# Optimization experiments

Hardware: AMD Instinct MI355X
Metric: run time of the kernel (lower is better)

Reference implementation:

```python
import jax, jax.numpy as jnp
import numpy as np

N_NODES = 100000
N_EDGES = 1600000
D_IN = 128
H1 = 128           # hidden_channels
H2 = int(H1 * 0.6) # 76, per int(hidden_channels * 0.6)
D_OUT = 64


def setup_inputs() -> dict:
    key = jax.random.key(0)
    ks = jax.random.split(key, 12)
    def lin(k, fan_in, fan_out):
        # torch Linear default init: U(-1/sqrt(fan_in), 1/sqrt(fan_in)); stored as [in, out]
        bound = 1.0 / np.sqrt(fan_in)
        return jax.random.uniform(k, (fan_in, fan_out), jnp.float32, -bound, bound)
    x = jax.random.normal(ks[0], (N_NODES, D_IN), jnp.float32)
    edge_index = jax.random.randint(ks[1], (2, N_EDGES), 0, N_NODES, dtype=jnp.int64)
    return {
        "x": x,
        "edge_index": edge_index,
        "Wl1": lin(ks[2], D_IN, H1),  "Wr1": lin(ks[3], D_IN, H1),
        "b1": jnp.zeros((H1,), jnp.float32),
        "Wl2": lin(ks[4], H1, H2),    "Wr2": lin(ks[5], H1, H2),
        "b2": jnp.zeros((H2,), jnp.float32),
        "Wl3": lin(ks[6], H2, D_OUT), "Wr3": lin(ks[7], H2, D_OUT),
        "b3": jnp.zeros((D_OUT,), jnp.float32),
    }


def reference(x, edge_index, Wl1, Wr1, b1, Wl2, Wr2, b2, Wl3, Wr3, b3):
    src, dst = edge_index[0], edge_index[1]
    n = x.shape[0]
    # in-degree of each target node (mean aggregation denominator), clamped to 1
    deg = jax.ops.segment_sum(jnp.ones_like(src, dtype=x.dtype), dst, num_segments=n)
    inv_deg = (1.0 / jnp.maximum(deg, 1.0))[:, None]

    def sage(h, Wl, Wr, b):
        # gather source features, scatter-add to targets, mean, then dual linear
        agg = jax.ops.segment_sum(h[src], dst, num_segments=n) * inv_deg
        return agg @ Wl + h @ Wr + b  # lin_l(mean_j x_j) + lin_r(x_i) + bias

    h = jax.nn.relu(sage(x, Wl1, Wr1, b1))
    h = jax.nn.relu(sage(h, Wl2, Wr2, b2))
    return sage(h, Wl3, Wr3, b3)
```

## Files before the change

kernel.cpp:

```cpp
#include <hip/hip_runtime.h>
#include <hip/hip_bf16.h>
#include <cstdint>
#include <cstddef>


typedef __attribute__((ext_vector_type(8))) short bf16x8;
typedef __attribute__((ext_vector_type(4))) float f32x4;

__device__ __forceinline__ short f2bf(float f) {
  uint32_t u = __builtin_bit_cast(uint32_t, f);
  u += 0x7fffu + ((u >> 16) & 1u);
  return (short)(u >> 16);
}
__device__ __forceinline__ float bflo(uint32_t u) {
  union { uint32_t i; float f; } v; v.i = u << 16; return v.f;
}
__device__ __forceinline__ float bfhi(uint32_t u) {
  union { uint32_t i; float f; } v; v.i = u & 0xffff0000u; return v.f;
}

__global__ void k_detect(const int* __restrict__ ei, int* __restrict__ flag, int E) {
  int t = threadIdx.x;
  int stride = E / 4096; if (stride < 1) stride = 1;
  int found = 0;
  for (int i = t; i < 4096; i += 256) {
    long long e = (long long)i * stride;
    if (e < E && ei[2 * e + 1] != 0) found = 1;
  }
  if (found) atomicOr(flag, 1);
}

__device__ __forceinline__ int edge_val(const int* ei, int is64, size_t pos) {
  return is64 ? ei[2 * pos] : ei[pos];
}

#define GPART 256

__global__ __launch_bounds__(256)
void k_bhist(const int* __restrict__ ei, const int* __restrict__ flag,
             int* __restrict__ hist, int E, int NB, int CPB) {
  __shared__ int lh[1024];
  int g = blockIdx.x, t = threadIdx.x;
  for (int b = t; b < NB; b += 256) lh[b] = 0;
  __syncthreads();
  int is64 = (*flag == 0);
  int e0 = g * CPB, e1 = min(e0 + CPB, E);
  for (int e = e0 + t; e < e1; e += 256) {
    int d = edge_val(ei, is64, (size_t)E + e);
    atomicAdd(&lh[d >> 7], 1);
  }
  __syncthreads();
  for (int b = t; b < NB; b += 256) hist[(size_t)g * NB + b] = lh[b];
}

__global__ void k_csum(const int* __restrict__ hist, int* __restrict__ total,
                       int NB, int G) {
  int b = blockIdx.x, t = threadIdx.x;
  int s = 0;
  for (int g = t; g < G; g += 64) s += hist[(size_t)g * NB + b];
  for (int off = 32; off; off >>= 1) s += __shfl_down(s, off);
  if (t == 0) total[b] = s;
}

__global__ void k_bscan(const int* __restrict__ total, int* __restrict__ bbase,
                        int NB) {
  __shared__ int sh[1024];
  int t = threadIdx.x;
  int v = (t < NB) ? total[t] : 0;
  sh[t] = v; __syncthreads();
  for (int off = 1; off < 1024; off <<= 1) {
    int x = (t >= off) ? sh[t - off] : 0;
    __syncthreads();
    sh[t] += x;
    __syncthreads();
  }
  if (t < NB) bbase[t] = sh[t] - v;
  if (t == NB - 1) bbase[NB] = sh[t];
}

__global__ void k_coff(int* __restrict__ hist, const int* __restrict__ bbase,
                       int NB, int G) {
  int b = blockIdx.x, t = threadIdx.x;
  int carry = bbase[b];
  for (int g0 = 0; g0 < G; g0 += 64) {
    int v = hist[(size_t)(g0 + t) * NB + b];
    int incl = v;
    #pragma unroll
    for (int off = 1; off < 64; off <<= 1) {
      int x = __shfl_up(incl, off);
      if (t >= off) incl += x;
    }
    hist[(size_t)(g0 + t) * NB + b] = carry + incl - v;
    carry += __shfl(incl, 63);
  }
}

__global__ __launch_bounds__(256)
void k_bscatter(const int* __restrict__ ei, const int* __restrict__ flag,
                const int* __restrict__ off, uint32_t* __restrict__ staging,
                int E, int NB, int CPB) {
  __shared__ int lcur[1024];
  int g = blockIdx.x, t = threadIdx.x;
  for (int b = t; b < NB; b += 256) lcur[b] = off[(size_t)g * NB + b];
  __syncthreads();
  int is64 = (*flag == 0);
  int e0 = g * CPB, e1 = min(e0 + CPB, E);
  for (int e = e0 + t; e < e1; e += 256) {
    int s = edge_val(ei, is64, (size_t)e);
    int d = edge_val(ei, is64, (size_t)E + e);
    int p = atomicAdd(&lcur[d >> 7], 1);
    staging[p] = ((uint32_t)(d & 127) << 25) | (uint32_t)s;
  }
}

#define LDSCAP 12288
__global__ __launch_bounds__(256)
void k_bfinal(const uint32_t* __restrict__ staging, const int* __restrict__ bbase,
              int* __restrict__ row_start, int* __restrict__ sorted_src,
              int N, int NB, int E) {
  __shared__ uint32_t ent[LDSCAP];
  __shared__ int cnt[128];
  __shared__ int pre[128];
  int b = blockIdx.x, t = threadIdx.x;
  int base = bbase[b], sz = bbase[b + 1] - base;
  int n0 = b << 7;
  if (t < 128) cnt[t] = 0;
  __syncthreads();
  bool fit = (sz <= LDSCAP);
  if (fit) {
    for (int i = t; i < sz; i += 256) {
      uint32_t u = staging[base + i];
      ent[i] = u;
      atomicAdd(&cnt[u >> 25], 1);
    }
  } else {
    for (int i = t; i < sz; i += 256)
      atomicAdd(&cnt[staging[base + i] >> 25], 1);
  }
  __syncthreads();
  if (t < 128) pre[t] = cnt[t];
  __syncthreads();
  #pragma unroll
  for (int off = 1; off < 128; off <<= 1) {
    int x = (t < 128 && t >= off) ? pre[t - off] : 0;
    __syncthreads();
    if (t < 128) pre[t] += x;
    __syncthreads();
  }
  int nn = N - n0; if (nn > 128) nn = 128;
  if (t < 128) {
    int ex = pre[t] - cnt[t];
    if (t < nn) row_start[n0 + t] = base + ex;
    cnt[t] = ex;
  }
  if (b == NB - 1 && t == 0) row_start[N] = E;
  __syncthreads();
  if (fit) {
    for (int i = t; i < sz; i += 256) {
      uint32_t u = ent[i];
      int p = atomicAdd(&cnt[u >> 25], 1);
      sorted_src[base + p] = (int)(u & 0x1FFFFFFu);
    }
  } else {
    for (int i = t; i < sz; i += 256) {
      uint32_t u = staging[base + i];
      int p = atomicAdd(&cnt[u >> 25], 1);
      sorted_src[base + p] = (int)(u & 0x1FFFFFFu);
    }
  }
}

__global__ void k_wprep(const float* __restrict__ Wl, const float* __restrict__ Wr,
                        short* __restrict__ Wt, int K, int H, int Hp, int Kp, int NP) {
  int idx = blockIdx.x * 256 + threadIdx.x;
  if (idx >= NP * Kp) return;
  int c = idx / Kp, k = idx - c * Kp;
  float v = 0.f;
  if (k < K) {
    if (c < H) v = Wl[(size_t)k * H + c];
    else if (c >= Hp && c - Hp < H) v = Wr[(size_t)k * H + (c - Hp)];
  }
  Wt[idx] = f2bf(v);
}

#define PK 136

template<int MODE, int NKS>
__global__ __launch_bounds__(256)
void k_gemm_mfma(const void* __restrict__ Av, const short* __restrict__ Wt,
                 const float* __restrict__ bias, short* __restrict__ P,
                 float* __restrict__ Q, int M, int K, int H, int Hp, int NP) {
  __shared__ short As[128][PK];
  const int Kp = NKS * 32;
  int t = threadIdx.x;
  int m0 = blockIdx.x * 128;

  if (MODE == 0) {
    const float* A = (const float*)Av;
    for (int idx = t; idx < 128 * (128 / 4); idx += 256) {
      int row = idx >> 5, c4 = (idx & 31) << 2;
      int gr = m0 + row;
      float4 v = make_float4(0.f, 0.f, 0.f, 0.f);
      if (gr < M) v = *(const float4*)(A + (size_t)gr * K + c4);
      uint2 pk;
      pk.x = (uint32_t)(uint16_t)f2bf(v.x) | ((uint32_t)(uint16_t)f2bf(v.y) << 16);
      pk.y = (uint32_t)(uint16_t)f2bf(v.z) | ((uint32_t)(uint16_t)f2bf(v.w) << 16);
      *(uint2*)&As[row][c4] = pk;
    }
  } else if (MODE == 1) {
    const short* A = (const short*)Av;
    for (int idx = t; idx < 128 * (128 / 4); idx += 256) {
      int row = idx >> 5, c4 = (idx & 31) << 2;
      int gr = m0 + row;
      uint2 v = make_uint2(0u, 0u);
      if (gr < M) v = *(const uint2*)(A + (size_t)gr * K + c4);
      *(uint2*)&As[row][c4] = v;
    }
  } else {
    const short* A = (const short*)Av;
    for (int idx = t; idx < 128 * 48; idx += 256) {
      int row = idx / 48, c2 = idx - row * 48;
      int k = c2 * 2;
      int gr = m0 + row;
      uint32_t v = 0u;
      if (gr < M && k < K) v = *(const uint32_t*)(A + (size_t)gr * K + k);
      *(uint32_t*)&As[row][k] = v;
    }
  }

  int wv = __builtin_amdgcn_readfirstlane(t >> 6);
  int lane = t & 63;
  int ncf_total = NP >> 4;
  int qd = ncf_total >> 2, rm = ncf_total & 3;
  int cf0 = wv * qd + (wv < rm ? wv : rm);
  int myncf = qd + (wv < rm ? 1 : 0);

  int lrow = lane & 15;
  int lk8 = (lane >> 4) * 8;

  bf16x8 b[4][NKS];
  #pragma unroll
  for (int cf = 0; cf < 4; cf++) {
    if (cf < myncf) {
      int col = (cf0 + cf) * 16 + lrow;
      #pragma unroll
      for (int ks = 0; ks < NKS; ks++)
        b[cf][ks] = *(const bf16x8*)(Wt + (size_t)col * Kp + ks * 32 + lk8);
    }
  }

  __syncthreads();

  for (int rf = 0; rf < 8; ++rf) {
    bf16x8 a[NKS];
    #pragma unroll
    for (int ks = 0; ks < NKS; ks++)
      a[ks] = *(const bf16x8*)&As[rf * 16 + lrow][ks * 32 + lk8];
    f32x4 acc[4];
    #pragma unroll
    for (int cf = 0; cf < 4; cf++) acc[cf] = (f32x4){0.f, 0.f, 0.f, 0.f};
    #pragma unroll
    for (int ks = 0; ks < NKS; ks++) {
      #pragma unroll
      for (int cf = 0; cf < 4; cf++) {
        if (cf < myncf)
          acc[cf] = __builtin_amdgcn_mfma_f32_16x16x32_bf16(a[ks], b[cf][ks], acc[cf], 0, 0, 0);
      }
    }
    int r0 = m0 + rf * 16 + (lane >> 4) * 4;
    #pragma unroll
    for (int cf = 0; cf < 4; cf++) {
      if (cf < myncf) {
        int c = (cf0 + cf) * 16 + lrow;
        bool isP = c < Hp;
        int cc = isP ? c : c - Hp;
        if (cc < H) {
          #pragma unroll
          for (int rg = 0; rg < 4; rg++) {
            int rr = r0 + rg;
            if (rr < M) {
              float v = acc[cf][rg];
              if (isP) P[(size_t)rr * H + cc] = f2bf(v);
              else     Q[(size_t)rr * H + cc] = v + bias[cc];
            }
          }
        }
      }
    }
  }
}

template<int RELU, int PACK, int OUTBF16>
__global__ __launch_bounds__(256)
void k_agg(const short* __restrict__ P, const float* Q,
           const int* __restrict__ rs, const int* __restrict__ srcs,
           void* out, int N, int H) {
  int wave = threadIdx.x >> 6;
  int lane = threadIdx.x & 63;
  int node = blockIdx.x * 4 + wave;
  if (node >= N) return;
  int start = rs[node];
  int deg = rs[node + 1] - start;
  int c = lane * PACK;
  bool act = c < H;
  float a0 = 0.f, a1 = 0.f;
  const int* sp = srcs + start;

  for (int base = 0; base < deg; base += 64) {
    int cnt = deg - base; if (cnt > 64) cnt = 64;
    int myidx = (lane < cnt) ? sp[base + lane] : 0;
    int e = 0;
    int nfull = cnt & ~3;
    for (; e < nfull; e += 4) {
      int s0 = __shfl(myidx, e);
      int s1 = __shfl(myidx, e + 1);
      int s2 = __shfl(myidx, e + 2);
      int s3 = __shfl(myidx, e + 3);
      if (act) {
        if (PACK == 2) {
          uint32_t u0 = *(const uint32_t*)(P + (size_t)s0 * H + c);
          uint32_t u1 = *(const uint32_t*)(P + (size_t)s1 * H + c);
          uint32_t u2 = *(const uint32_t*)(P + (size_t)s2 * H + c);
          uint32_t u3 = *(const uint32_t*)(P + (size_t)s3 * H + c);
          a0 += bflo(u0); a1 += bfhi(u0);
          a0 += bflo(u1); a1 += bfhi(u1);
          a0 += bflo(u2); a1 += bfhi(u2);
          a0 += bflo(u3); a1 += bfhi(u3);
        } else {
          uint32_t u0 = *(const uint16_t*)(P + (size_t)s0 * H + c);
          uint32_t u1 = *(const uint16_t*)(P + (size_t)s1 * H + c);
          uint32_t u2 = *(const uint16_t*)(P + (size_t)s2 * H + c);
          uint32_t u3 = *(const uint16_t*)(P + (size_t)s3 * H + c);
          a0 += bflo(u0) + bflo(u1) + bflo(u2) + bflo(u3);
        }
      }
    }
    for (; e < cnt; ++e) {
      int s0 = __shfl(myidx, e);
      if (act) {
        if (PACK == 2) {
          uint32_t u0 = *(const uint32_t*)(P + (size_t)s0 * H + c);
          a0 += bflo(u0); a1 += bfhi(u0);
        } else {
          uint32_t u0 = *(const uint16_t*)(P + (size_t)s0 * H + c);
          a0 += bflo(u0);
        }
      }
    }
  }

  if (!act) return;
  float scale = 1.f / (float)(deg > 0 ? deg : 1);
  size_t o = (size_t)node * H + c;
  if (PACK == 2) {
    float2 q = *(const float2*)(Q + o);
    float v0 = a0 * scale + q.x;
    float v1 = a1 * scale + q.y;
    if (RELU) { v0 = fmaxf(v0, 0.f); v1 = fmaxf(v1, 0.f); }
    if (OUTBF16) {
      uint32_t pk = (uint32_t)(uint16_t)f2bf(v0) | ((uint32_t)(uint16_t)f2bf(v1) << 16);
      *(uint32_t*)((short*)out + o) = pk;
    } else {
      float2 r; r.x = v0; r.y = v1;
      *(float2*)((float*)out + o) = r;
    }
  } else {
    float v0 = a0 * scale + Q[o];
    if (RELU) v0 = fmaxf(v0, 0.f);
    if (OUTBF16) ((short*)out)[o] = f2bf(v0);
    else ((float*)out)[o] = v0;
  }
}

extern "C" void kernel_launch(void* const* d_in, const int* in_sizes, int n_in,
                              void* d_out, int out_size, void* d_ws, size_t ws_size,
                              hipStream_t stream) {
  const float* x   = (const float*)d_in[0];
  const int*   ei  = (const int*)d_in[1];
  const float* Wl1 = (const float*)d_in[2];
  const float* Wr1 = (const float*)d_in[3];
  const float* b1  = (const float*)d_in[4];
  const float* Wl2 = (const float*)d_in[5];
  const float* Wr2 = (const float*)d_in[6];
  const float* b2  = (const float*)d_in[7];
  const float* Wl3 = (const float*)d_in[8];
  const float* Wr3 = (const float*)d_in[9];
  const float* b3  = (const float*)d_in[10];

  const int DIN = 128;
  const int N  = in_sizes[0] / DIN;
  const int E  = in_sizes[1] / 2;
  const int H1 = in_sizes[4];
  const int H2 = in_sizes[7];
  const int H3 = in_sizes[10];
  const int Hp1 = 128, Hp2 = 80, Hp3 = 64;
  const int Kp12 = 128, Kp3 = 96;
  const int NB = (N + 127) >> 7;
  const int G = GPART;
  const int CPB = (E + G - 1) / G;

  char* w = (char*)d_ws;
  auto alloc = [&](size_t bytes) {
    char* p = w;
    w += (bytes + 255) & ~(size_t)255;
    return p;
  };
  short* bufP  = (short*)alloc((size_t)N * 128 * 2);
  short* bufH1 = (short*)alloc((size_t)N * 128 * 2);
  short* bufH2 = (short*)alloc((size_t)N * 80 * 2);
  float* bufB  = (float*)alloc((size_t)N * 128 * 4);
  float* bufC  = (float*)alloc((size_t)N * 80 * 4);
  short* Wt1   = (short*)alloc((size_t)256 * 128 * 2);
  short* Wt2   = (short*)alloc((size_t)160 * 128 * 2);
  short* Wt3   = (short*)alloc((size_t)128 * 96 * 2);
  int* row_start = (int*)alloc((size_t)(N + 1) * 4);
  int* hist      = (int*)alloc((size_t)G * NB * 4);
  int* total     = (int*)alloc((size_t)NB * 4);
  int* bbase     = (int*)alloc((size_t)(NB + 1) * 4);
  uint32_t* staging = (uint32_t*)alloc((size_t)E * 4);
  int* sorted    = (int*)alloc((size_t)E * 4);
  int* flag      = (int*)alloc(256);

  k_wprep<<<(256 * 128 + 255) / 256, 256, 0, stream>>>(Wl1, Wr1, Wt1, DIN, H1, Hp1, Kp12, 2 * Hp1);
  k_wprep<<<(160 * 128 + 255) / 256, 256, 0, stream>>>(Wl2, Wr2, Wt2, H1, H2, Hp2, Kp12, 2 * Hp2);
  k_wprep<<<(128 * 96 + 255) / 256, 256, 0, stream>>>(Wl3, Wr3, Wt3, H2, H3, Hp3, Kp3, 2 * Hp3);

  hipMemsetAsync(flag, 0, 4, stream);
  k_detect<<<1, 256, 0, stream>>>(ei, flag, E);
  k_bhist<<<G, 256, 0, stream>>>(ei, flag, hist, E, NB, CPB);
  k_csum<<<NB, 64, 0, stream>>>(hist, total, NB, G);
  k_bscan<<<1, 1024, 0, stream>>>(total, bbase, NB);
  k_coff<<<NB, 64, 0, stream>>>(hist, bbase, NB, G);
  k_bscatter<<<G, 256, 0, stream>>>(ei, flag, hist, staging, E, NB, CPB);
  k_bfinal<<<NB, 256, 0, stream>>>(staging, bbase, row_start, sorted, N, NB, E);

  int gemmGrid = (N + 127) / 128;
  int aggGrid = (N + 3) / 4;

  k_gemm_mfma<0, 4><<<gemmGrid, 256, 0, stream>>>(x, Wt1, b1, bufP, bufB, N, DIN, H1, Hp1, 2 * Hp1);
  k_agg<1, 2, 1><<<aggGrid, 256, 0, stream>>>(bufP, bufB, row_start, sorted, bufH1, N, H1);

  k_gemm_mfma<1, 4><<<gemmGrid, 256, 0, stream>>>(bufH1, Wt2, b2, bufP, bufC, N, H1, H2, Hp2, 2 * Hp2);
  k_agg<1, 2, 1><<<aggGrid, 256, 0, stream>>>(bufP, bufC, row_start, sorted, bufH2, N, H2);

  k_gemm_mfma<2, 3><<<gemmGrid, 256, 0, stream>>>(bufH2, Wt3, b3, bufP, bufB, N, H2, H3, Hp3, 2 * Hp3);
  k_agg<0, 1, 0><<<aggGrid, 256, 0, stream>>>(bufP, bufB, row_start, sorted, d_out, N, H3);
}
```

Measured before the change: 430.4 us.

## Rewrite dual-linear GEMM without LDS and store self-term in bf16

Replaces the LDS-staged 128-row GEMM with a register-only kernel. Each wave loads its A rows straight from global memory and computes two 16-column fragments, using a 2D grid over row tiles and column groups. The self-term (Q plus bias) for layers 1 and 2 is now written and read back in bf16 instead of fp32, cutting memory traffic between the GEMM and aggregation kernels at some precision cost. The layer-2 output is stored with a padded stride of 96, so the layer-3 GEMM can use aligned vector loads. Those padding columns are never written, which is a risk if the workspace holds NaNs.

```diff
diff --git a/kernel.cpp b/kernel.cpp
--- a/kernel.cpp
+++ b/kernel.cpp
@@ -183,105 +183,94 @@
   Wt[idx] = f2bf(v);
 }
 
-#define PK 136
-
-template<int MODE, int NKS>
-__global__ __launch_bounds__(256)
-void k_gemm_mfma(const void* __restrict__ Av, const short* __restrict__ Wt,
-                 const float* __restrict__ bias, short* __restrict__ P,
-                 float* __restrict__ Q, int M, int K, int H, int Hp, int NP) {
-  __shared__ short As[128][PK];
+template<int MODE, int NKS, int QBF16>
+__global__ __launch_bounds__(256, 4)
+void k_gemm2(const void* __restrict__ Av, const short* __restrict__ Wt,
+             const float* __restrict__ bias, short* __restrict__ P,
+             void* __restrict__ Qv, int M, int lda, int H, int Hp, int F) {
   const int Kp = NKS * 32;
   int t = threadIdx.x;
-  int m0 = blockIdx.x * 128;
-
-  if (MODE == 0) {
-    const float* A = (const float*)Av;
-    for (int idx = t; idx < 128 * (128 / 4); idx += 256) {
-      int row = idx >> 5, c4 = (idx & 31) << 2;
-      int gr = m0 + row;
-      float4 v = make_float4(0.f, 0.f, 0.f, 0.f);
-      if (gr < M) v = *(const float4*)(A + (size_t)gr * K + c4);
-      uint2 pk;
-      pk.x = (uint32_t)(uint16_t)f2bf(v.x) | ((uint32_t)(uint16_t)f2bf(v.y) << 16);
-      pk.y = (uint32_t)(uint16_t)f2bf(v.z) | ((uint32_t)(uint16_t)f2bf(v.w) << 16);
-      *(uint2*)&As[row][c4] = pk;
-    }
-  } else if (MODE == 1) {
-    const short* A = (const short*)Av;
-    for (int idx = t; idx < 128 * (128 / 4); idx += 256) {
-      int row = idx >> 5, c4 = (idx & 31) << 2;
-      int gr = m0 + row;
-      uint2 v = make_uint2(0u, 0u);
-      if (gr < M) v = *(const uint2*)(A + (size_t)gr * K + c4);
-      *(uint2*)&As[row][c4] = v;
-    }
-  } else {
-    const short* A = (const short*)Av;
-    for (int idx = t; idx < 128 * 48; idx += 256) {
-      int row = idx / 48, c2 = idx - row * 48;
-      int k = c2 * 2;
-      int gr = m0 + row;
-      uint32_t v = 0u;
-      if (gr < M && k < K) v = *(const uint32_t*)(A + (size_t)gr * K + k);
-      *(uint32_t*)&As[row][k] = v;
-    }
-  }
-
-  int wv = __builtin_amdgcn_readfirstlane(t >> 6);
-  int lane = t & 63;
-  int ncf_total = NP >> 4;
-  int qd = ncf_total >> 2, rm = ncf_total & 3;
-  int cf0 = wv * qd + (wv < rm ? wv : rm);
-  int myncf = qd + (wv < rm ? 1 : 0);
-
-  int lrow = lane & 15;
-  int lk8 = (lane >> 4) * 8;
-
-  bf16x8 b[4][NKS];
+  int wv = t >> 6, lane = t & 63;
+  int lrow = lane & 15, lk8 = (lane >> 4) * 8;
+  int m0 = blockIdx.x * 64;
+  int f0 = blockIdx.y * 8 + wv * 2;
+  int nf = F - f0; nf = nf < 0 ? 0 : (nf > 2 ? 2 : nf);
+  if (nf == 0) return;
+
+  bf16x8 b[2][NKS];
+  float bia[2];
+  int ccol[2]; bool isPc[2]; bool cok[2];
   #pragma unroll
-  for (int cf = 0; cf < 4; cf++) {
-    if (cf < myncf) {
-      int col = (cf0 + cf) * 16 + lrow;
+  for (int cf = 0; cf < 2; cf++) {
+    int c = (f0 + cf) * 16 + lrow;
+    bool p = c < Hp;
+    int cc = p ? c : c - Hp;
+    ccol[cf] = cc; isPc[cf] = p;
+    cok[cf] = (cf < nf) && (cc < H);
+    bia[cf] = (cok[cf] && !p) ? bias[cc] : 0.f;
+    if (cf < nf) {
+      const short* wp = Wt + (size_t)c * Kp + lk8;
       #pragma unroll
       for (int ks = 0; ks < NKS; ks++)
-        b[cf][ks] = *(const bf16x8*)(Wt + (size_t)col * Kp + ks * 32 + lk8);
-    }
-  }
-
-  __syncthreads();
-
-  for (int rf = 0; rf < 8; ++rf) {
+        b[cf][ks] = *(const bf16x8*)(wp + ks * 32);
+    }
+  }
+
+  #pragma unroll
+  for (int rf = 0; rf < 4; rf++) {
+    int arow = m0 + rf * 16 + lrow;
+    bool rok = arow < M;
     bf16x8 a[NKS];
-    #pragma unroll
-    for (int ks = 0; ks < NKS; ks++)
-      a[ks] = *(const bf16x8*)&As[rf * 16 + lrow][ks * 32 + lk8];
-    f32x4 acc[4];
-    #pragma unroll
-    for (int cf = 0; cf < 4; cf++) acc[cf] = (f32x4){0.f, 0.f, 0.f, 0.f};
+    if (MODE == 0) {
+      const float* ap = (const float*)Av + (size_t)arow * lda + lk8;
+      #pragma unroll
+      for (int ks = 0; ks < NKS; ks++) {
+        if (rok) {
+          float4 v0 = *(const float4*)(ap + ks * 32);
+          float4 v1 = *(const float4*)(ap + ks * 32 + 4);
+          bf16x8 r;
+          r[0] = f2bf(v0.x); r[1] = f2bf(v0.y); r[2] = f2bf(v0.z); r[3] = f2bf(v0.w);
+          r[4] = f2bf(v1.x); r[5] = f2bf(v1.y); r[6] = f2bf(v1.z); r[7] = f2bf(v1.w);
+          a[ks] = r;
+        } else {
+          a[ks] = (bf16x8){0, 0, 0, 0, 0, 0, 0, 0};
+        }
+      }
+    } else {
+      const short* ap = (const short*)Av + (size_t)arow * lda + lk8;
+      #pragma unroll
+      for (int ks = 0; ks < NKS; ks++)
+        a[ks] = rok ? *(const bf16x8*)(ap + ks * 32)
+                    : (bf16x8){0, 0, 0, 0, 0, 0, 0, 0};
+    }
+
+    f32x4 acc[2];
+    acc[0] = (f32x4){0.f, 0.f, 0.f, 0.f};
+    acc[1] = (f32x4){0.f, 0.f, 0.f, 0.f};
     #pragma unroll
     for (int ks = 0; ks < NKS; ks++) {
       #pragma unroll
-      for (int cf = 0; cf < 4; cf++) {
-        if (cf < myncf)
+      for (int cf = 0; cf < 2; cf++) {
+        if (cf < nf)
           acc[cf] = __builtin_amdgcn_mfma_f32_16x16x32_bf16(a[ks], b[cf][ks], acc[cf], 0, 0, 0);
       }
     }
-    int r0 = m0 + rf * 16 + (lane >> 4) * 4;
+
+    int rbase = m0 + rf * 16 + (lane >> 4) * 4;
     #pragma unroll
-    for (int cf = 0; cf < 4; cf++) {
-      if (cf < myncf) {
-        int c = (cf0 + cf) * 16 + lrow;
-        bool isP = c < Hp;
-        int cc = isP ? c : c - Hp;
-        if (cc < H) {
-          #pragma unroll
-          for (int rg = 0; rg < 4; rg++) {
-            int rr = r0 + rg;
-            if (rr < M) {
-              float v = acc[cf][rg];
-              if (isP) P[(size_t)rr * H + cc] = f2bf(v);
-              else     Q[(size_t)rr * H + cc] = v + bias[cc];
+    for (int cf = 0; cf < 2; cf++) {
+      if (cok[cf]) {
+        #pragma unroll
+        for (int rg = 0; rg < 4; rg++) {
+          int rr = rbase + rg;
+          if (rr < M) {
+            float v = acc[cf][rg];
+            if (isPc[cf]) {
+              P[(size_t)rr * H + ccol[cf]] = f2bf(v);
+            } else {
+              v += bia[cf];
+              if (QBF16) ((short*)Qv)[(size_t)rr * H + ccol[cf]] = f2bf(v);
+              else       ((float*)Qv)[(size_t)rr * H + ccol[cf]] = v;
             }
           }
         }
@@ -290,11 +279,11 @@
   }
 }
 
-template<int RELU, int PACK, int OUTBF16>
+template<int RELU, int PACK, int OUTBF16, int QBF16>
 __global__ __launch_bounds__(256)
-void k_agg(const short* __restrict__ P, const float* Q,
+void k_agg(const short* __restrict__ P, const void* Q,
            const int* __restrict__ rs, const int* __restrict__ srcs,
-           void* out, int N, int H) {
+           void* out, int N, int H, int HSo) {
   int wave = threadIdx.x >> 6;
   int lane = threadIdx.x & 63;
   int node = blockIdx.x * 4 + wave;
@@ -351,24 +340,35 @@
 
   if (!act) return;
   float scale = 1.f / (float)(deg > 0 ? deg : 1);
-  size_t o = (size_t)node * H + c;
+  size_t oq = (size_t)node * H + c;
+  size_t oo = (size_t)node * HSo + c;
   if (PACK == 2) {
-    float2 q = *(const float2*)(Q + o);
-    float v0 = a0 * scale + q.x;
-    float v1 = a1 * scale + q.y;
+    float q0, q1;
+    if (QBF16) {
+      uint32_t qu = *(const uint32_t*)((const short*)Q + oq);
+      q0 = bflo(qu); q1 = bfhi(qu);
+    } else {
+      float2 q = *(const float2*)((const float*)Q + oq);
+      q0 = q.x; q1 = q.y;
+    }
+    float v0 = a0 * scale + q0;
+    float v1 = a1 * scale + q1;
     if (RELU) { v0 = fmaxf(v0, 0.f); v1 = fmaxf(v1, 0.f); }
     if (OUTBF16) {
       uint32_t pk = (uint32_t)(uint16_t)f2bf(v0) | ((uint32_t)(uint16_t)f2bf(v1) << 16);
-      *(uint32_t*)((short*)out + o) = pk;
+      *(uint32_t*)((short*)out + oo) = pk;
     } else {
       float2 r; r.x = v0; r.y = v1;
-      *(float2*)((float*)out + o) = r;
+      *(float2*)((float*)out + oo) = r;
     }
   } else {
-    float v0 = a0 * scale + Q[o];
+    float q0;
+    if (QBF16) q0 = bflo(*(const uint16_t*)((const short*)Q + oq));
+    else       q0 = ((const float*)Q)[oq];
+    float v0 = a0 * scale + q0;
     if (RELU) v0 = fmaxf(v0, 0.f);
-    if (OUTBF16) ((short*)out)[o] = f2bf(v0);
-    else ((float*)out)[o] = v0;
+    if (OUTBF16) ((short*)out)[oo] = f2bf(v0);
+    else ((float*)out)[oo] = v0;
   }
 }
 
@@ -407,9 +407,10 @@
   };
   short* bufP  = (short*)alloc((size_t)N * 128 * 2);
   short* bufH1 = (short*)alloc((size_t)N * 128 * 2);
-  short* bufH2 = (short*)alloc((size_t)N * 80 * 2);
-  float* bufB  = (float*)alloc((size_t)N * 128 * 4);
-  float* bufC  = (float*)alloc((size_t)N * 80 * 4);
+  short* bufH2 = (short*)alloc((size_t)N * 96 * 2);
+  short* q1    = (short*)alloc((size_t)N * 128 * 2);
+  short* q2    = (short*)alloc((size_t)N * 76 * 2);
+  float* q3    = (float*)alloc((size_t)N * 64 * 4);
   short* Wt1   = (short*)alloc((size_t)256 * 128 * 2);
   short* Wt2   = (short*)alloc((size_t)160 * 128 * 2);
   short* Wt3   = (short*)alloc((size_t)128 * 96 * 2);
@@ -434,15 +435,15 @@
   k_bscatter<<<G, 256, 0, stream>>>(ei, flag, hist, staging, E, NB, CPB);
   k_bfinal<<<NB, 256, 0, stream>>>(staging, bbase, row_start, sorted, N, NB, E);
 
-  int gemmGrid = (N + 127) / 128;
+  int gx = (N + 63) / 64;
   int aggGrid = (N + 3) / 4;
 
-  k_gemm_mfma<0, 4><<<gemmGrid, 256, 0, stream>>>(x, Wt1, b1, bufP, bufB, N, DIN, H1, Hp1, 2 * Hp1);
-  k_agg<1, 2, 1><<<aggGrid, 256, 0, stream>>>(bufP, bufB, row_start, sorted, bufH1, N, H1);
-
-  k_gemm_mfma<1, 4><<<gemmGrid, 256, 0, stream>>>(bufH1, Wt2, b2, bufP, bufC, N, H1, H2, Hp2, 2 * Hp2);
-  k_agg<1, 2, 1><<<aggGrid, 256, 0, stream>>>(bufP, bufC, row_start, sorted, bufH2, N, H2);
-
-  k_gemm_mfma<2, 3><<<gemmGrid, 256, 0, stream>>>(bufH2, Wt3, b3, bufP, bufB, N, H2, H3, Hp3, 2 * Hp3);
-  k_agg<0, 1, 0><<<aggGrid, 256, 0, stream>>>(bufP, bufB, row_start, sorted, d_out, N, H3);
-}
+  k_gemm2<0, 4, 1><<<dim3(gx, 2), 256, 0, stream>>>(x, Wt1, b1, bufP, q1, N, DIN, H1, Hp1, 16);
+  k_agg<1, 2, 1, 1><<<aggGrid, 256, 0, stream>>>(bufP, q1, row_start, sorted, bufH1, N, H1, 128);
+
+  k_gemm2<1, 4, 1><<<dim3(gx, 2), 256, 0, stream>>>(bufH1, Wt2, b2, bufP, q2, N, Kp12, H2, Hp2, 10);
+  k_agg<1, 2, 1, 1><<<aggGrid, 256, 0, stream>>>(bufP, q2, row_start, sorted, bufH2, N, H2, 96);
+
+  k_gemm2<1, 3, 0><<<dim3(gx, 1), 256, 0, stream>>>(bufH2, Wt3, b3, bufP, q3, N, Kp3, H3, Hp3, 8);
+  k_agg<0, 1, 0, 0><<<aggGrid, 256, 0, stream>>>(bufP, q3, row_start, sorted, d_out, N, H3, 64);
+}
```

Measured after the change: 360.8 us. 16.2% less time.
